# Optimization experiments

Hardware: AMD Instinct MI355X
Metric: run time of the kernel (lower is better)

Reference implementation:

```python
import jax, jax.numpy as jnp
import numpy as np

H, W = 64, 64
B, P, F = 8, 512, 512
EXPAND = 0.02      # bbox expansion for soft silhouette (NDC units), DIB-R default
MULT = 1000.0      # DIB-R coordinate multiplier
DELTA = 7000.0     # soft prob falloff in multiplier-scaled squared units, DIB-R default
EPS = 1e-10


def setup_inputs() -> dict:
    key = jax.random.key(0)
    k1, k2, k3 = jax.random.split(key, 3)
    verts = 0.5 * jax.random.normal(k1, (B, P, 3), dtype=jnp.float32)
    faces = jax.random.randint(k2, (B, F, 3), 0, P, dtype=jnp.int32)
    colors = jax.random.uniform(k3, (B, P, 3), dtype=jnp.float32)
    camera_rot = jnp.tile(jnp.eye(3, dtype=jnp.float32)[None], (B, 1, 1))
    camera_pos = jnp.tile(jnp.array([0.0, 0.0, 3.0], dtype=jnp.float32)[None], (B, 1))
    fov_factor = 2.7475  # 1 / tan(fovy/2), fovy ~ 0.7 rad, aspect 1
    camera_proj = jnp.array([[fov_factor], [fov_factor], [-1.0]], dtype=jnp.float32)
    return {"verts": verts, "faces": faces, "camera_rot": camera_rot,
            "camera_pos": camera_pos, "camera_proj": camera_proj, "colors": colors}


def _render_one(verts_p3, faces_f3, rot_33, pos_3, proj_31, colors_p3):
    # --- perspective_projection (pixel2mesh convention: p' = rot^T (p - pos)) ---
    pcam = (verts_p3 - pos_3[None, :]) @ rot_33.T                 # [P,3] camera frame
    xy3 = pcam * proj_31.reshape(3)[None, :]
    xy = xy3[:, :2] / xy3[:, 2:3]                                  # [P,2] NDC
    tri3d = pcam[faces_f3]                                         # [F,3,3]
    tri2d = xy[faces_f3]                                           # [F,3,2]
    normal = jnp.cross(tri3d[:, 1] - tri3d[:, 0], tri3d[:, 2] - tri3d[:, 0])  # [F,3]
    normalz = normal[:, 2]
    normal1 = normal / (jnp.linalg.norm(normal, axis=1, keepdims=True) + 1e-12)
    # per-face vertex colors + hard-mask channel -> [F,3,4] (== color_1xfx12)
    cmask = jnp.ones((faces_f3.shape[0], 3, 1), dtype=colors_p3.dtype)
    cfeat = jnp.concatenate([colors_p3[faces_f3], cmask], axis=2)

    # --- linear_rasterizer: pixel grid in NDC ---
    xs = (2.0 * jnp.arange(W, dtype=jnp.float32) + 1.0 - W) / W
    ys = (H - 2.0 * jnp.arange(H, dtype=jnp.float32) - 1.0) / H
    x0 = xs[None, :, None]                                         # [1,W,1]
    y0 = ys[:, None, None]                                         # [H,1,1]
    ax, ay = tri2d[:, 0, 0], tri2d[:, 0, 1]
    bx, by = tri2d[:, 1, 0], tri2d[:, 1, 1]
    cx, cy = tri2d[:, 2, 0], tri2d[:, 2, 1]
    det = (by - cy) * (ax - cx) + (cx - bx) * (ay - cy)            # [F]
    det_safe = jnp.where(jnp.abs(det) < EPS, EPS, det)
    w0 = ((by - cy) * (x0 - cx) + (cx - bx) * (y0 - cy)) / det_safe  # [H,W,F]
    w1 = ((cy - ay) * (x0 - cx) + (ax - cx) * (y0 - cy)) / det_safe
    w2 = 1.0 - w0 - w1
    z = w0 * tri3d[:, 0, 2] + w1 * tri3d[:, 1, 2] + w2 * tri3d[:, 2, 2]  # [H,W,F]
    covered = (w0 >= 0) & (w1 >= 0) & (w2 >= 0)
    valid = covered & (normalz > 0) & (jnp.abs(det) > EPS)
    # hard z-buffer: camera looks along -z, so nearest face has max z
    zbuf = jnp.where(valid, z, -1e10)
    best = jnp.argmax(zbuf, axis=-1)                               # [H,W]
    anyv = jnp.any(valid, axis=-1)
    gw = lambda w: jnp.take_along_axis(w, best[..., None], axis=-1)[..., 0]
    g0, g1, g2 = gw(w0), gw(w1), gw(w2)
    cb = cfeat[best]                                               # [H,W,3,4]
    feat = (g0[..., None] * cb[..., 0, :] + g1[..., None] * cb[..., 1, :]
            + g2[..., None] * cb[..., 2, :])
    imfeat = jnp.where(anyv[..., None], feat, 0.0)                 # [H,W,4]

    # --- soft silhouette probability ---
    def seg_d2(px, py, qx, qy):
        vx, vy = qx - px, qy - py
        t = jnp.clip(((x0 - px) * vx + (y0 - py) * vy)
                     / (vx * vx + vy * vy + 1e-12), 0.0, 1.0)
        dx, dy = x0 - (px + t * vx), y0 - (py + t * vy)
        return dx * dx + dy * dy
    d2 = jnp.minimum(jnp.minimum(seg_d2(ax, ay, bx, by), seg_d2(bx, by, cx, cy)),
                     seg_d2(cx, cy, ax, ay))
    d2 = jnp.where(covered, 0.0, d2)                               # inside -> 0
    xmin = jnp.minimum(jnp.minimum(ax, bx), cx) - EXPAND
    xmax = jnp.maximum(jnp.maximum(ax, bx), cx) + EXPAND
    ymin = jnp.minimum(jnp.minimum(ay, by), cy) - EXPAND
    ymax = jnp.maximum(jnp.maximum(ay, by), cy) + EXPAND
    in_bbox = (x0 >= xmin) & (x0 <= xmax) & (y0 >= ymin) & (y0 <= ymax)
    contrib = jnp.where(in_bbox, jnp.exp(-d2 * (MULT * MULT) / DELTA), 0.0)
    improb = 1.0 - jnp.prod(1.0 - contrib, axis=-1, keepdims=True)  # [H,W,1]
    return imfeat, improb, normal1


def reference(verts, faces, camera_rot, camera_pos, camera_proj, colors):
    imfeat, improb, normal1 = jax.vmap(_render_one, in_axes=(0, 0, 0, 0, None, 0))(
        verts, faces, camera_rot, camera_pos, camera_proj, colors)
    imrender = imfeat[..., :3]     # [B,H,W,3]
    hardmask = imfeat[..., 3:]     # [B,H,W,1]
    return imrender, improb, normal1, hardmask
```

## Files before the change

### kernel.cpp

```cpp
#include <hip/hip_runtime.h>
#include <math.h>

#define NB 8
#define NP 512
#define NF 512
#define NH 64
#define NW 64
#define FEXPAND 0.02f
#define FEPS 1e-10f

#define IMG_OFF 0
#define PROB_OFF (NB*NH*NW*3)
#define NRM_OFF  (PROB_OFF + NB*NH*NW)
#define MASK_OFF (NRM_OFF + NB*NF*3)

__device__ __forceinline__ void bary(float e0x, float e0y, float e1x, float e1y,
                                     float det_safe, float cx, float cy,
                                     float x, float y,
                                     float& w0, float& w1, float& w2,
                                     float& dxc, float& dyc) {
  dxc = x - cx; dyc = y - cy;
  float n0 = __fadd_rn(__fmul_rn(e0x, dxc), __fmul_rn(e0y, dyc));
  float n1 = __fadd_rn(__fmul_rn(e1x, dxc), __fmul_rn(e1y, dyc));
  w0 = __fdiv_rn(n0, det_safe);
  w1 = __fdiv_rn(n1, det_safe);
  w2 = __fsub_rn(__fsub_rn(1.0f, w0), w1);
}

#define CHUNK 128

__global__ __launch_bounds__(256, 8) void render_all(
    const float* __restrict__ verts, const int* __restrict__ faces,
    const float* __restrict__ rot, const float* __restrict__ pos,
    const float* __restrict__ proj, const float* __restrict__ colors,
    float* __restrict__ out)
{
  __shared__ __align__(16) float sf[CHUNK][36];
  int tid  = threadIdx.x;
  int wave = tid >> 6;
  int lane = tid & 63;
  int fg   = lane >> 4;
  int pl   = lane & 15;
  int gp   = blockIdx.x * 16 + pl;
  int b    = blockIdx.x >> 8;
  int rem  = gp & 4095;
  int iy   = rem >> 6, ix = rem & 63;
  float x = (2.0f*ix + 1.0f - 64.0f) * (1.0f/64.0f);
  float y = (64.0f - 2.0f*iy - 1.0f) * (1.0f/64.0f);
  bool norm_write = ((blockIdx.x & 255) == 0);

  float bestz = -1e10f;
  int   bestf = 0;
  float bw0 = 0.0f, bw1 = 0.0f, bw2 = 0.0f;
  float prod  = 1.0f;
  int   anyv  = 0;

  for (int c0 = 0; c0 < NF; c0 += CHUNK) {
    __syncthreads();
    if (tid < CHUNK) {
      int fidx = c0 + tid;
      int t = b * NF + fidx;
      float p0 = proj[0], p1 = proj[1], p2 = proj[2];
      float R0=rot[b*9+0],R1=rot[b*9+1],R2=rot[b*9+2];
      float R3=rot[b*9+3],R4=rot[b*9+4],R5=rot[b*9+5];
      float R6=rot[b*9+6],R7=rot[b*9+7],R8=rot[b*9+8];
      float ppx=pos[b*3+0], ppy=pos[b*3+1], ppz=pos[b*3+2];
      int idxs[3] = { faces[t*3+0], faces[t*3+1], faces[t*3+2] };
      float X[3],Y[3],Z[3],SX[3],SY[3];
#pragma unroll
      for (int k = 0; k < 3; ++k) {
        const float* v = verts + ((size_t)b*NP + idxs[k])*3;
        float dx = v[0]-ppx, dy = v[1]-ppy, dz = v[2]-ppz;
        float pcx = __fadd_rn(__fadd_rn(__fmul_rn(R0,dx),__fmul_rn(R1,dy)),__fmul_rn(R2,dz));
        float pcy = __fadd_rn(__fadd_rn(__fmul_rn(R3,dx),__fmul_rn(R4,dy)),__fmul_rn(R5,dz));
        float pcz = __fadd_rn(__fadd_rn(__fmul_rn(R6,dx),__fmul_rn(R7,dy)),__fmul_rn(R8,dz));
        X[k]=pcx; Y[k]=pcy; Z[k]=pcz;
        float dn = __fmul_rn(pcz, p2);
        SX[k] = __fdiv_rn(__fmul_rn(pcx, p0), dn);
        SY[k] = __fdiv_rn(__fmul_rn(pcy, p1), dn);
      }
      float e1x=X[1]-X[0], e1y=Y[1]-Y[0], e1z=Z[1]-Z[0];
      float e2x=X[2]-X[0], e2y=Y[2]-Y[0], e2z=Z[2]-Z[0];
      float nzel = __fsub_rn(__fmul_rn(e1x,e2y), __fmul_rn(e1y,e2x));
      if (norm_write) {
        float m0 = __fmul_rn(e1z, e2y); float nxf = __fmaf_rn(e1y, e2z, -m0);
        float m1 = __fmul_rn(e1x, e2z); float nyf = __fmaf_rn(e1z, e2x, -m1);
        float m2 = __fmul_rn(e1y, e2x); float nzf = __fmaf_rn(e1x, e2y, -m2);
        float nn = __fsqrt_rn(__fadd_rn(__fadd_rn(__fmul_rn(nxf,nxf),__fmul_rn(nyf,nyf)),
                                        __fmul_rn(nzf,nzf)));
        float den = __fadd_rn(nn, 1e-12f);
        out[NRM_OFF + (size_t)t*3+0] = __fdiv_rn(nxf, den);
        out[NRM_OFF + (size_t)t*3+1] = __fdiv_rn(nyf, den);
        out[NRM_OFF + (size_t)t*3+2] = __fdiv_rn(nzf, den);
      }
      float ax=SX[0],ay=SY[0],bx=SX[1],by=SY[1],cx=SX[2],cy=SY[2];
      float det = __fadd_rn(__fmul_rn(__fsub_rn(by,cy),__fsub_rn(ax,cx)),
                            __fmul_rn(__fsub_rn(cx,bx),__fsub_rn(ay,cy)));
      float det_safe = (fabsf(det) < FEPS) ? FEPS : det;
      float validf = ((nzel > 0.0f) && (fabsf(det) > FEPS)) ? 1.0f : 0.0f;
      float* d = sf[tid];
      d[0]=by-cy; d[1]=cx-bx; d[2]=cy-ay; d[3]=ax-cx;
      d[4]=cx; d[5]=cy; d[6]=det_safe; d[7]=validf;
      d[8]=Z[0]; d[9]=Z[1]; d[10]=Z[2]; d[11]=0.0f;
      d[12]=fminf(fminf(ax,bx),cx)-FEXPAND; d[13]=fmaxf(fmaxf(ax,bx),cx)+FEXPAND;
      d[14]=fminf(fminf(ay,by),cy)-FEXPAND; d[15]=fmaxf(fmaxf(ay,by),cy)+FEXPAND;
      d[16]=ax; d[17]=ay; d[18]=bx; d[19]=by;
      float vx=bx-ax, vy=by-ay;
      d[20]=vx; d[21]=vy; d[22]=1.0f/(vx*vx+vy*vy+1e-12f); d[23]=0.0f;
      vx=cx-bx; vy=cy-by;
      d[24]=vx; d[25]=vy; d[26]=1.0f/(vx*vx+vy*vy+1e-12f); d[27]=0.0f;
      vx=ax-cx; vy=ay-cy;
      d[28]=vx; d[29]=vy; d[30]=1.0f/(vx*vx+vy*vy+1e-12f); d[31]=0.0f;
      d[32]=0.0f; d[33]=0.0f; d[34]=0.0f; d[35]=0.0f;
    }
    __syncthreads();

    for (int j = 0; j < 8; ++j) {
      int l = wave*32 + (j << 2) + fg;
      int g = c0 + l;
      const float4* fl = reinterpret_cast<const float4*>(sf[l]);
      float4 bb = fl[3];
      bool inb = (x >= bb.x) && (x <= bb.y) && (y >= bb.z) && (y <= bb.w);
      if (!inb) continue;
      float4 E  = fl[0];
      float4 C  = fl[1];
      float4 Zv = fl[2];
      float w0,w1,w2,dxc,dyc;
      bary(E.x,E.y,E.z,E.w, C.z, C.x, C.y, x, y, w0,w1,w2,dxc,dyc);
      bool covered = (w0 >= 0.0f) && (w1 >= 0.0f) && (w2 >= 0.0f);
      bool valid   = covered && (C.w > 0.5f);
      float z = __fadd_rn(__fadd_rn(__fmul_rn(w0,Zv.x), __fmul_rn(w1,Zv.y)),
                          __fmul_rn(w2,Zv.z));
      float zval = valid ? z : -1e10f;
      if (zval > bestz) { bestz = zval; bestf = g; bw0 = w0; bw1 = w1; bw2 = w2; }
      anyv |= (int)valid;
      float4 A4 = fl[4];
      float4 S1 = fl[5], S2 = fl[6], S3 = fl[7];
      float dxa = x - A4.x, dya = y - A4.y;
      float t = fminf(fmaxf((dxa*S1.x + dya*S1.y)*S1.z, 0.0f), 1.0f);
      float rx = dxa - t*S1.x, ry = dya - t*S1.y;
      float d2 = rx*rx + ry*ry;
      float dxb = x - A4.z, dyb = y - A4.w;
      t = fminf(fmaxf((dxb*S2.x + dyb*S2.y)*S2.z, 0.0f), 1.0f);
      rx = dxb - t*S2.x; ry = dyb - t*S2.y;
      d2 = fminf(d2, rx*rx + ry*ry);
      t = fminf(fmaxf((dxc*S3.x + dyc*S3.y)*S3.z, 0.0f), 1.0f);
      rx = dxc - t*S3.x; ry = dyc - t*S3.y;
      d2 = fminf(d2, rx*rx + ry*ry);
      d2 = covered ? 0.0f : d2;
      prod *= (1.0f - __expf(d2 * -142.85714285714286f));
    }
  }

  for (int off = 16; off < 64; off <<= 1) {
    float oz = __shfl_xor(bestz, off, 64);
    int   of = __shfl_xor(bestf, off, 64);
    float op = __shfl_xor(prod,  off, 64);
    int   oa = __shfl_xor(anyv,  off, 64);
    float o0 = __shfl_xor(bw0,   off, 64);
    float o1 = __shfl_xor(bw1,   off, 64);
    float o2 = __shfl_xor(bw2,   off, 64);
    if (oz > bestz || (oz == bestz && of < bestf)) {
      bestz = oz; bestf = of; bw0 = o0; bw1 = o1; bw2 = o2;
    }
    prod *= op;
    anyv |= oa;
  }

  __syncthreads();
  float* comb = &sf[0][0];
  if (fg == 0) {
    float* cc = comb + (size_t)(wave*16 + pl)*8;
    cc[0]=bestz; cc[1]=__int_as_float(bestf); cc[2]=prod; cc[3]=anyv?1.0f:0.0f;
    cc[4]=bw0; cc[5]=bw1; cc[6]=bw2; cc[7]=0.0f;
  }
  __syncthreads();
  if (tid < 16) {
    const float* c0p = comb + (size_t)tid*8;
    float bz = c0p[0]; int bf = __float_as_int(c0p[1]);
    float pr = c0p[2]; int av = (c0p[3] != 0.0f);
    float w0 = c0p[4], w1 = c0p[5], w2 = c0p[6];
    for (int s = 1; s < 4; ++s) {
      const float* cs = comb + (size_t)(s*16 + tid)*8;
      float oz = cs[0]; int of = __float_as_int(cs[1]);
      if (oz > bz || (oz == bz && of < bf)) { bz = oz; bf = of; w0 = cs[4]; w1 = cs[5]; w2 = cs[6]; }
      pr *= cs[2];
      av |= (cs[3] != 0.0f);
    }
    int t = b * NF + bf;
    const int* fi = faces + (size_t)t*3;
    const float* cb = colors + (size_t)b*NP*3;
    int i0 = fi[0], i1 = fi[1], i2 = fi[2];
    float fr  = w0*cb[i0*3+0] + w1*cb[i1*3+0] + w2*cb[i2*3+0];
    float fgc = w0*cb[i0*3+1] + w1*cb[i1*3+1] + w2*cb[i2*3+1];
    float fb  = w0*cb[i0*3+2] + w1*cb[i1*3+2] + w2*cb[i2*3+2];
    float fa  = __fadd_rn(__fadd_rn(w0, w1), w2);
    int gpp = blockIdx.x * 16 + tid;
    out[IMG_OFF + (size_t)gpp*3 + 0] = av ? fr  : 0.0f;
    out[IMG_OFF + (size_t)gpp*3 + 1] = av ? fgc : 0.0f;
    out[IMG_OFF + (size_t)gpp*3 + 2] = av ? fb  : 0.0f;
    out[PROB_OFF + gpp] = 1.0f - pr;
    out[MASK_OFF + gpp] = av ? fa : 0.0f;
  }
}

extern "C" void kernel_launch(void* const* d_in, const int* in_sizes, int n_in,
                              void* d_out, int out_size, void* d_ws, size_t ws_size,
                              hipStream_t stream) {
  const float* verts  = (const float*)d_in[0];
  const int*   faces  = (const int*)  d_in[1];
  const float* rot    = (const float*)d_in[2];
  const float* pos    = (const float*)d_in[3];
  const float* proj   = (const float*)d_in[4];
  const float* colors = (const float*)d_in[5];
  float* out = (float*)d_out;
  (void)d_ws; (void)ws_size;

  hipLaunchKernelGGL(render_all, dim3(NB*NH*NW/16), dim3(256), 0, stream,
                     verts, faces, rot, pos, proj, colors, out);
}
```

Baseline: 107.4 us.

## Use 8x8 pixel tiles per 1024-thread block with per-wave face-split and wave-uniform bbox skip

```diff
diff --git a/kernel.cpp b/kernel.cpp
--- a/kernel.cpp
+++ b/kernel.cpp
@@ -27,166 +27,147 @@
   w2 = __fsub_rn(__fsub_rn(1.0f, w0), w1);
 }
 
-#define CHUNK 128
-
-__global__ __launch_bounds__(256, 8) void render_all(
+__global__ __launch_bounds__(1024, 8) void render_all(
     const float* __restrict__ verts, const int* __restrict__ faces,
     const float* __restrict__ rot, const float* __restrict__ pos,
     const float* __restrict__ proj, const float* __restrict__ colors,
     float* __restrict__ out)
 {
-  __shared__ __align__(16) float sf[CHUNK][36];
+  __shared__ __align__(16) float smem[NF*20];
   int tid  = threadIdx.x;
+  int b    = blockIdx.x >> 6;
+  int tile = blockIdx.x & 63;
   int wave = tid >> 6;
   int lane = tid & 63;
-  int fg   = lane >> 4;
-  int pl   = lane & 15;
-  int gp   = blockIdx.x * 16 + pl;
-  int b    = blockIdx.x >> 8;
-  int rem  = gp & 4095;
-  int iy   = rem >> 6, ix = rem & 63;
+  int ix = (tile & 7)*8 + (lane & 7);
+  int iy = (tile >> 3)*8 + (lane >> 3);
   float x = (2.0f*ix + 1.0f - 64.0f) * (1.0f/64.0f);
   float y = (64.0f - 2.0f*iy - 1.0f) * (1.0f/64.0f);
-  bool norm_write = ((blockIdx.x & 255) == 0);
+
+  if (tid < NF) {
+    int t = b * NF + tid;
+    float p0 = proj[0], p1 = proj[1], p2 = proj[2];
+    float R0=rot[b*9+0],R1=rot[b*9+1],R2=rot[b*9+2];
+    float R3=rot[b*9+3],R4=rot[b*9+4],R5=rot[b*9+5];
+    float R6=rot[b*9+6],R7=rot[b*9+7],R8=rot[b*9+8];
+    float ppx=pos[b*3+0], ppy=pos[b*3+1], ppz=pos[b*3+2];
+    int idxs[3] = { faces[t*3+0], faces[t*3+1], faces[t*3+2] };
+    float X[3],Y[3],Z[3],SX[3],SY[3];
+#pragma unroll
+    for (int k = 0; k < 3; ++k) {
+      const float* v = verts + ((size_t)b*NP + idxs[k])*3;
+      float dx = v[0]-ppx, dy = v[1]-ppy, dz = v[2]-ppz;
+      float pcx = __fadd_rn(__fadd_rn(__fmul_rn(R0,dx),__fmul_rn(R1,dy)),__fmul_rn(R2,dz));
+      float pcy = __fadd_rn(__fadd_rn(__fmul_rn(R3,dx),__fmul_rn(R4,dy)),__fmul_rn(R5,dz));
+      float pcz = __fadd_rn(__fadd_rn(__fmul_rn(R6,dx),__fmul_rn(R7,dy)),__fmul_rn(R8,dz));
+      X[k]=pcx; Y[k]=pcy; Z[k]=pcz;
+      float dn = __fmul_rn(pcz, p2);
+      SX[k] = __fdiv_rn(__fmul_rn(pcx, p0), dn);
+      SY[k] = __fdiv_rn(__fmul_rn(pcy, p1), dn);
+    }
+    float e1x=X[1]-X[0], e1y=Y[1]-Y[0], e1z=Z[1]-Z[0];
+    float e2x=X[2]-X[0], e2y=Y[2]-Y[0], e2z=Z[2]-Z[0];
+    float nzel = __fsub_rn(__fmul_rn(e1x,e2y), __fmul_rn(e1y,e2x));
+    if (tile == 0) {
+      float m0 = __fmul_rn(e1z, e2y); float nxf = __fmaf_rn(e1y, e2z, -m0);
+      float m1 = __fmul_rn(e1x, e2z); float nyf = __fmaf_rn(e1z, e2x, -m1);
+      float m2 = __fmul_rn(e1y, e2x); float nzf = __fmaf_rn(e1x, e2y, -m2);
+      float nn = __fsqrt_rn(__fadd_rn(__fadd_rn(__fmul_rn(nxf,nxf),__fmul_rn(nyf,nyf)),
+                                      __fmul_rn(nzf,nzf)));
+      float den = __fadd_rn(nn, 1e-12f);
+      out[NRM_OFF + (size_t)t*3+0] = __fdiv_rn(nxf, den);
+      out[NRM_OFF + (size_t)t*3+1] = __fdiv_rn(nyf, den);
+      out[NRM_OFF + (size_t)t*3+2] = __fdiv_rn(nzf, den);
+    }
+    float ax=SX[0],ay=SY[0],bx=SX[1],by=SY[1],cx=SX[2],cy=SY[2];
+    float det = __fadd_rn(__fmul_rn(__fsub_rn(by,cy),__fsub_rn(ax,cx)),
+                          __fmul_rn(__fsub_rn(cx,bx),__fsub_rn(ay,cy)));
+    float det_safe = (fabsf(det) < FEPS) ? FEPS : det;
+    float validf = ((nzel > 0.0f) && (fabsf(det) > FEPS)) ? 1.0f : 0.0f;
+    float* d = &smem[tid*20];
+    d[0]=ax; d[1]=ay; d[2]=bx; d[3]=by;
+    d[4]=cx; d[5]=cy; d[6]=det_safe; d[7]=validf;
+    d[8]=Z[0]; d[9]=Z[1]; d[10]=Z[2];
+    float vx=bx-ax, vy=by-ay;
+    d[11]=1.0f/(vx*vx+vy*vy+1e-12f);
+    d[12]=fminf(fminf(ax,bx),cx)-FEXPAND; d[13]=fmaxf(fmaxf(ax,bx),cx)+FEXPAND;
+    d[14]=fminf(fminf(ay,by),cy)-FEXPAND; d[15]=fmaxf(fmaxf(ay,by),cy)+FEXPAND;
+    vx=cx-bx; vy=cy-by;
+    d[16]=1.0f/(vx*vx+vy*vy+1e-12f);
+    vx=ax-cx; vy=ay-cy;
+    d[17]=1.0f/(vx*vx+vy*vy+1e-12f);
+    d[18]=0.0f; d[19]=0.0f;
+  }
+  __syncthreads();
 
   float bestz = -1e10f;
   int   bestf = 0;
   float bw0 = 0.0f, bw1 = 0.0f, bw2 = 0.0f;
   float prod  = 1.0f;
-  int   anyv  = 0;
-
-  for (int c0 = 0; c0 < NF; c0 += CHUNK) {
-    __syncthreads();
-    if (tid < CHUNK) {
-      int fidx = c0 + tid;
-      int t = b * NF + fidx;
-      float p0 = proj[0], p1 = proj[1], p2 = proj[2];
-      float R0=rot[b*9+0],R1=rot[b*9+1],R2=rot[b*9+2];
-      float R3=rot[b*9+3],R4=rot[b*9+4],R5=rot[b*9+5];
-      float R6=rot[b*9+6],R7=rot[b*9+7],R8=rot[b*9+8];
-      float ppx=pos[b*3+0], ppy=pos[b*3+1], ppz=pos[b*3+2];
-      int idxs[3] = { faces[t*3+0], faces[t*3+1], faces[t*3+2] };
-      float X[3],Y[3],Z[3],SX[3],SY[3];
-#pragma unroll
-      for (int k = 0; k < 3; ++k) {
-        const float* v = verts + ((size_t)b*NP + idxs[k])*3;
-        float dx = v[0]-ppx, dy = v[1]-ppy, dz = v[2]-ppz;
-        float pcx = __fadd_rn(__fadd_rn(__fmul_rn(R0,dx),__fmul_rn(R1,dy)),__fmul_rn(R2,dz));
-        float pcy = __fadd_rn(__fadd_rn(__fmul_rn(R3,dx),__fmul_rn(R4,dy)),__fmul_rn(R5,dz));
-        float pcz = __fadd_rn(__fadd_rn(__fmul_rn(R6,dx),__fmul_rn(R7,dy)),__fmul_rn(R8,dz));
-        X[k]=pcx; Y[k]=pcy; Z[k]=pcz;
-        float dn = __fmul_rn(pcz, p2);
-        SX[k] = __fdiv_rn(__fmul_rn(pcx, p0), dn);
-        SY[k] = __fdiv_rn(__fmul_rn(pcy, p1), dn);
+
+  float4 bb = *(const float4*)&smem[wave*20 + 12];
+  for (int j = 0; j < 32; ++j) {
+    int f = (j << 4) + wave;
+    float4 bbn = bb;
+    if (j < 31) bbn = *(const float4*)&smem[(f + 16)*20 + 12];
+    bool inb = (x >= bb.x) && (x <= bb.y) && (y >= bb.z) && (y <= bb.w);
+    if (__any(inb)) {
+      const float* r = &smem[f*20];
+      float4 q0 = *(const float4*)(r);
+      float4 q1 = *(const float4*)(r + 4);
+      float4 q2 = *(const float4*)(r + 8);
+      float iBC = r[16], iCA = r[17];
+      float ax=q0.x, ay=q0.y, bxx=q0.z, byy=q0.w, cx=q1.x, cy=q1.y;
+      float e0x=__fsub_rn(byy,cy), e0y=__fsub_rn(cx,bxx);
+      float e1x=__fsub_rn(cy,ay),  e1y=__fsub_rn(ax,cx);
+      float w0,w1,w2,dxc,dyc;
+      bary(e0x,e0y,e1x,e1y, q1.z, cx, cy, x, y, w0,w1,w2,dxc,dyc);
+      bool covered = (w0 >= 0.0f) && (w1 >= 0.0f) && (w2 >= 0.0f);
+      bool valid   = covered && (q1.w > 0.5f);
+      float z = __fadd_rn(__fadd_rn(__fmul_rn(w0,q2.x), __fmul_rn(w1,q2.y)),
+                          __fmul_rn(w2,q2.z));
+      if (inb) {
+        float zval = valid ? z : -1e10f;
+        if (zval > bestz) { bestz = zval; bestf = f; bw0 = w0; bw1 = w1; bw2 = w2; }
+        float dxa = x - ax, dya = y - ay;
+        float vABx=__fsub_rn(bxx,ax), vABy=__fsub_rn(byy,ay);
+        float t1 = fminf(fmaxf((dxa*vABx + dya*vABy)*q2.w, 0.0f), 1.0f);
+        float rx = dxa - t1*vABx, ry = dya - t1*vABy;
+        float d2 = rx*rx + ry*ry;
+        float dxb = x - bxx, dyb = y - byy;
+        float vBCx=__fsub_rn(cx,bxx), vBCy=__fsub_rn(cy,byy);
+        t1 = fminf(fmaxf((dxb*vBCx + dyb*vBCy)*iBC, 0.0f), 1.0f);
+        rx = dxb - t1*vBCx; ry = dyb - t1*vBCy;
+        d2 = fminf(d2, rx*rx + ry*ry);
+        float vCAx=__fsub_rn(ax,cx), vCAy=__fsub_rn(ay,cy);
+        t1 = fminf(fmaxf((dxc*vCAx + dyc*vCAy)*iCA, 0.0f), 1.0f);
+        rx = dxc - t1*vCAx; ry = dyc - t1*vCAy;
+        d2 = fminf(d2, rx*rx + ry*ry);
+        d2 = covered ? 0.0f : d2;
+        prod *= (1.0f - __expf(d2 * -142.85714285714286f));
       }
-      float e1x=X[1]-X[0], e1y=Y[1]-Y[0], e1z=Z[1]-Z[0];
-      float e2x=X[2]-X[0], e2y=Y[2]-Y[0], e2z=Z[2]-Z[0];
-      float nzel = __fsub_rn(__fmul_rn(e1x,e2y), __fmul_rn(e1y,e2x));
-      if (norm_write) {
-        float m0 = __fmul_rn(e1z, e2y); float nxf = __fmaf_rn(e1y, e2z, -m0);
-        float m1 = __fmul_rn(e1x, e2z); float nyf = __fmaf_rn(e1z, e2x, -m1);
-        float m2 = __fmul_rn(e1y, e2x); float nzf = __fmaf_rn(e1x, e2y, -m2);
-        float nn = __fsqrt_rn(__fadd_rn(__fadd_rn(__fmul_rn(nxf,nxf),__fmul_rn(nyf,nyf)),
-                                        __fmul_rn(nzf,nzf)));
-        float den = __fadd_rn(nn, 1e-12f);
-        out[NRM_OFF + (size_t)t*3+0] = __fdiv_rn(nxf, den);
-        out[NRM_OFF + (size_t)t*3+1] = __fdiv_rn(nyf, den);
-        out[NRM_OFF + (size_t)t*3+2] = __fdiv_rn(nzf, den);
-      }
-      float ax=SX[0],ay=SY[0],bx=SX[1],by=SY[1],cx=SX[2],cy=SY[2];
-      float det = __fadd_rn(__fmul_rn(__fsub_rn(by,cy),__fsub_rn(ax,cx)),
-                            __fmul_rn(__fsub_rn(cx,bx),__fsub_rn(ay,cy)));
-      float det_safe = (fabsf(det) < FEPS) ? FEPS : det;
-      float validf = ((nzel > 0.0f) && (fabsf(det) > FEPS)) ? 1.0f : 0.0f;
-      float* d = sf[tid];
-      d[0]=by-cy; d[1]=cx-bx; d[2]=cy-ay; d[3]=ax-cx;
-      d[4]=cx; d[5]=cy; d[6]=det_safe; d[7]=validf;
-      d[8]=Z[0]; d[9]=Z[1]; d[10]=Z[2]; d[11]=0.0f;
-      d[12]=fminf(fminf(ax,bx),cx)-FEXPAND; d[13]=fmaxf(fmaxf(ax,bx),cx)+FEXPAND;
-      d[14]=fminf(fminf(ay,by),cy)-FEXPAND; d[15]=fmaxf(fmaxf(ay,by),cy)+FEXPAND;
-      d[16]=ax; d[17]=ay; d[18]=bx; d[19]=by;
-      float vx=bx-ax, vy=by-ay;
-      d[20]=vx; d[21]=vy; d[22]=1.0f/(vx*vx+vy*vy+1e-12f); d[23]=0.0f;
-      vx=cx-bx; vy=cy-by;
-      d[24]=vx; d[25]=vy; d[26]=1.0f/(vx*vx+vy*vy+1e-12f); d[27]=0.0f;
-      vx=ax-cx; vy=ay-cy;
-      d[28]=vx; d[29]=vy; d[30]=1.0f/(vx*vx+vy*vy+1e-12f); d[31]=0.0f;
-      d[32]=0.0f; d[33]=0.0f; d[34]=0.0f; d[35]=0.0f;
-    }
-    __syncthreads();
-
-    for (int j = 0; j < 8; ++j) {
-      int l = wave*32 + (j << 2) + fg;
-      int g = c0 + l;
-      const float4* fl = reinterpret_cast<const float4*>(sf[l]);
-      float4 bb = fl[3];
-      bool inb = (x >= bb.x) && (x <= bb.y) && (y >= bb.z) && (y <= bb.w);
-      if (!inb) continue;
-      float4 E  = fl[0];
-      float4 C  = fl[1];
-      float4 Zv = fl[2];
-      float w0,w1,w2,dxc,dyc;
-      bary(E.x,E.y,E.z,E.w, C.z, C.x, C.y, x, y, w0,w1,w2,dxc,dyc);
-      bool covered = (w0 >= 0.0f) && (w1 >= 0.0f) && (w2 >= 0.0f);
-      bool valid   = covered && (C.w > 0.5f);
-      float z = __fadd_rn(__fadd_rn(__fmul_rn(w0,Zv.x), __fmul_rn(w1,Zv.y)),
-                          __fmul_rn(w2,Zv.z));
-      float zval = valid ? z : -1e10f;
-      if (zval > bestz) { bestz = zval; bestf = g; bw0 = w0; bw1 = w1; bw2 = w2; }
-      anyv |= (int)valid;
-      float4 A4 = fl[4];
-      float4 S1 = fl[5], S2 = fl[6], S3 = fl[7];
-      float dxa = x - A4.x, dya = y - A4.y;
-      float t = fminf(fmaxf((dxa*S1.x + dya*S1.y)*S1.z, 0.0f), 1.0f);
-      float rx = dxa - t*S1.x, ry = dya - t*S1.y;
-      float d2 = rx*rx + ry*ry;
-      float dxb = x - A4.z, dyb = y - A4.w;
-      t = fminf(fmaxf((dxb*S2.x + dyb*S2.y)*S2.z, 0.0f), 1.0f);
-      rx = dxb - t*S2.x; ry = dyb - t*S2.y;
-      d2 = fminf(d2, rx*rx + ry*ry);
-      t = fminf(fmaxf((dxc*S3.x + dyc*S3.y)*S3.z, 0.0f), 1.0f);
-      rx = dxc - t*S3.x; ry = dyc - t*S3.y;
-      d2 = fminf(d2, rx*rx + ry*ry);
-      d2 = covered ? 0.0f : d2;
-      prod *= (1.0f - __expf(d2 * -142.85714285714286f));
-    }
+    }
+    bb = bbn;
   }
 
-  for (int off = 16; off < 64; off <<= 1) {
-    float oz = __shfl_xor(bestz, off, 64);
-    int   of = __shfl_xor(bestf, off, 64);
-    float op = __shfl_xor(prod,  off, 64);
-    int   oa = __shfl_xor(anyv,  off, 64);
-    float o0 = __shfl_xor(bw0,   off, 64);
-    float o1 = __shfl_xor(bw1,   off, 64);
-    float o2 = __shfl_xor(bw2,   off, 64);
-    if (oz > bestz || (oz == bestz && of < bestf)) {
-      bestz = oz; bestf = of; bw0 = o0; bw1 = o1; bw2 = o2;
-    }
-    prod *= op;
-    anyv |= oa;
-  }
-
   __syncthreads();
-  float* comb = &sf[0][0];
-  if (fg == 0) {
-    float* cc = comb + (size_t)(wave*16 + pl)*8;
-    cc[0]=bestz; cc[1]=__int_as_float(bestf); cc[2]=prod; cc[3]=anyv?1.0f:0.0f;
-    cc[4]=bw0; cc[5]=bw1; cc[6]=bw2; cc[7]=0.0f;
-  }
+  float* comb = smem;
+  float* c = comb + (size_t)(wave*64 + lane)*7;
+  c[0]=bestz; c[1]=__int_as_float(bestf); c[2]=prod;
+  c[3]=bw0; c[4]=bw1; c[5]=bw2;
   __syncthreads();
-  if (tid < 16) {
-    const float* c0p = comb + (size_t)tid*8;
-    float bz = c0p[0]; int bf = __float_as_int(c0p[1]);
-    float pr = c0p[2]; int av = (c0p[3] != 0.0f);
-    float w0 = c0p[4], w1 = c0p[5], w2 = c0p[6];
-    for (int s = 1; s < 4; ++s) {
-      const float* cs = comb + (size_t)(s*16 + tid)*8;
+
+  if (tid < 64) {
+    const float* c0 = comb + (size_t)tid*7;
+    float bz = c0[0]; int bf = __float_as_int(c0[1]); float pr = c0[2];
+    float w0 = c0[3], w1 = c0[4], w2 = c0[5];
+    for (int s = 1; s < 16; ++s) {
+      const float* cs = comb + (size_t)(s*64 + tid)*7;
       float oz = cs[0]; int of = __float_as_int(cs[1]);
-      if (oz > bz || (oz == bz && of < bf)) { bz = oz; bf = of; w0 = cs[4]; w1 = cs[5]; w2 = cs[6]; }
+      if (oz > bz || (oz == bz && of < bf)) { bz = oz; bf = of; w0 = cs[3]; w1 = cs[4]; w2 = cs[5]; }
       pr *= cs[2];
-      av |= (cs[3] != 0.0f);
-    }
+    }
+    int av = (bz != -1e10f);
     int t = b * NF + bf;
     const int* fi = faces + (size_t)t*3;
     const float* cb = colors + (size_t)b*NP*3;
@@ -195,12 +176,12 @@
     float fgc = w0*cb[i0*3+1] + w1*cb[i1*3+1] + w2*cb[i2*3+1];
     float fb  = w0*cb[i0*3+2] + w1*cb[i1*3+2] + w2*cb[i2*3+2];
     float fa  = __fadd_rn(__fadd_rn(w0, w1), w2);
-    int gpp = blockIdx.x * 16 + tid;
-    out[IMG_OFF + (size_t)gpp*3 + 0] = av ? fr  : 0.0f;
-    out[IMG_OFF + (size_t)gpp*3 + 1] = av ? fgc : 0.0f;
-    out[IMG_OFF + (size_t)gpp*3 + 2] = av ? fb  : 0.0f;
-    out[PROB_OFF + gpp] = 1.0f - pr;
-    out[MASK_OFF + gpp] = av ? fa : 0.0f;
+    int gp = b*4096 + iy*64 + ix;
+    out[IMG_OFF + (size_t)gp*3 + 0] = av ? fr  : 0.0f;
+    out[IMG_OFF + (size_t)gp*3 + 1] = av ? fgc : 0.0f;
+    out[IMG_OFF + (size_t)gp*3 + 2] = av ? fb  : 0.0f;
+    out[PROB_OFF + gp] = 1.0f - pr;
+    out[MASK_OFF + gp] = av ? fa : 0.0f;
   }
 }
 
@@ -216,6 +197,6 @@
   float* out = (float*)d_out;
   (void)d_ws; (void)ws_size;
 
-  hipLaunchKernelGGL(render_all, dim3(NB*NH*NW/16), dim3(256), 0, stream,
+  hipLaunchKernelGGL(render_all, dim3(NB*64), dim3(1024), 0, stream,
                      verts, faces, rot, pos, proj, colors, out);
 }
```

Result: faster. 94.09 us (-12.4%).
